# Optimization experiments

Measured on AMD Instinct MI355X. Metric: run time of the kernel, lower is better.

## Reference

```python
import jax, jax.numpy as jnp
import numpy as np

B, N, M, K = 8, 4096, 32, 72
D = 6 + K
W_REG, W_CLS = 3.0, 1.0
SIMOTA_Q = 4
IOU_LEN = 15.0
EPS = 1e-12
BIG = 100000.0


def setup_inputs() -> dict:
    key = jax.random.key(0)
    k1, k2, k3, k4, k5, k6 = jax.random.split(key, 6)
    preds = jax.random.normal(k1, (B, N, D), jnp.float32)
    # pred x-offsets in pixel range
    preds = preds.at[..., 6:].set(jax.random.uniform(k2, (B, N, K), jnp.float32, 0.0, 800.0))
    tgt = jax.random.normal(k3, (B, M, D), jnp.float32) * 0.1
    tgt = tgt.at[..., 1].set(jax.random.randint(k4, (B, M), 0, 2).astype(jnp.float32))
    tgt = tgt.at[..., 2:5].set(jax.random.uniform(k5, (B, M, 3), jnp.float32) * jnp.array([800.0, 320.0, 3.14159], jnp.float32))
    # target x-offsets, some out-of-range -> invalid points
    tgt = tgt.at[..., 6:].set(jax.random.uniform(k6, (B, M, K), jnp.float32, -50.0, 850.0))
    masks = jax.random.uniform(jax.random.fold_in(key, 7), (B, M)) > 0.2
    return {"preds": preds, "targets": tgt, "masks": masks, "img_w": 800, "img_h": 320}


def _focal_cost(cls_logits, gt_labels, alpha=0.25, gamma=2.0):
    # cls_logits [B,N,2], gt_labels [B,M] int -> [B,N,M]
    p = jax.nn.sigmoid(cls_logits)
    neg = -jnp.log(1.0 - p + EPS) * (1.0 - alpha) * p ** gamma
    pos = -jnp.log(p + EPS) * alpha * (1.0 - p) ** gamma
    diff = pos - neg  # [B,N,2]
    idx = jnp.broadcast_to(gt_labels[:, None, :], (gt_labels.shape[0], cls_logits.shape[1], gt_labels.shape[1]))
    return jnp.take_along_axis(diff, idx, axis=2)


def _pairwise_line_iou(pred_x, tgt_x, img_w, length=IOU_LEN):
    # pred_x [B,N,K], tgt_x [B,M,K] -> [B,N,M]
    p = pred_x[:, :, None, :]
    t = tgt_x[:, None, :, :]
    ovr = jnp.minimum(p + length, t + length) - jnp.maximum(p - length, t - length)
    union = jnp.maximum(p + length, t + length) - jnp.minimum(p - length, t - length)
    invalid = (t < 0) | (t >= img_w)
    ovr = jnp.where(invalid, 0.0, ovr)
    union = jnp.where(invalid, 0.0, union)
    return ovr.sum(-1) / (union.sum(-1) + 1e-9)


def _cost(preds, targets, masks, img_w):
    # -> cost [B,N,M]
    pred_dx = preds[..., 6:]
    tgt_dx = targets[..., 6:]
    invalid = (tgt_dx < 0) | (tgt_dx >= img_w)  # [B,M,K]
    lengths = jnp.maximum((~invalid).sum(-1), 1)  # [B,M]
    d = jnp.abs(tgt_dx[:, None, :, :] - pred_dx[:, :, None, :])  # [B,N,M,K]
    d = jnp.where(invalid[:, None, :, :], 0.0, d)
    distances = d.sum(-1) / lengths[:, None, :].astype(preds.dtype)  # [B,N,M]
    max_d = jnp.maximum(distances.max(axis=(1, 2), keepdims=True), 1e-6)
    dist_s = 1.0 - distances / max_d + 0.01
    xy = jnp.linalg.norm(preds[:, :, None, 2:4] - targets[:, None, :, 2:4], axis=-1)
    xy_s = 1.0 - xy / jnp.maximum(xy.max(axis=(1, 2), keepdims=True), 1e-6) + 0.01
    th = jnp.abs(preds[:, :, None, 4] - targets[:, None, :, 4])
    th_s = 1.0 - th / jnp.maximum(th.max(axis=(1, 2), keepdims=True), 1e-6) + 0.01
    cls_cost = _focal_cost(preds[..., :2], targets[..., 1].astype(jnp.int32))
    cost = -((dist_s * xy_s * th_s) ** 2) * W_REG + cls_cost * W_CLS
    return jnp.where(masks[:, None, :], cost, BIG)


def _assign(cost, iou, masks):
    b, n, m = cost.shape
    ious = jnp.where(masks[:, None, :], iou, 0.0)
    ious = jnp.maximum(ious, 0.0)
    n_cand = min(SIMOTA_Q, n)
    topk_ious, _ = jax.lax.top_k(jnp.swapaxes(ious, 1, 2), n_cand)  # [B,M,q]
    dynamic_ks = jnp.clip(topk_ious.sum(-1).astype(jnp.int32), 1, n)  # [B,M]
    # since line-iou <= 1, dynamic_ks <= SIMOTA_Q -> static max_k = n_cand
    max_k = n_cand
    _, topk_idx = jax.lax.top_k(-jnp.swapaxes(cost, 1, 2), max_k)  # [B,M,max_k] smallest costs
    k_mask = jnp.arange(max_k)[None, None, :] < dynamic_ks[:, :, None]  # [B,M,max_k]
    bi = jnp.arange(b)[:, None, None]
    mi = jnp.arange(m)[None, :, None]
    mmT = jnp.zeros((b, m, n), cost.dtype).at[bi, mi, topk_idx].set(k_mask.astype(cost.dtype))
    matching = jnp.swapaxes(mmT, 1, 2)  # [B,N,M]
    matching = jnp.where(masks[:, None, :], matching, 0.0)
    matched_gt = matching.sum(-1)  # [B,N]
    conflict = matched_gt > 1.0
    cost_inf = jnp.where(matching == 0.0, jnp.inf, cost)
    min_idx = jnp.argmin(cost_inf, axis=2)  # [B,N]
    one_hot = jax.nn.one_hot(min_idx, m, dtype=cost.dtype)
    matching = jnp.where(conflict[:, :, None], one_hot, matching)
    assigned = matching.sum(-1) > 0.0
    matched_t = jnp.argmax(matching, axis=2)
    matched_t = jnp.where(assigned, matched_t, -1)
    return assigned, matched_t


def reference(preds, targets, masks, img_w, img_h):
    cost = _cost(preds, targets, masks, img_w)
    iou = _pairwise_line_iou(preds[..., 6:], targets[..., 6:], img_w)
    return _assign(cost, iou, masks)
```

## Files before the change

### kernel.cpp

```cpp
#include <hip/hip_runtime.h>
#include <stdint.h>

#define BB 8
#define NN 4096
#define MM 32
#define KK 72
#define DD 78
#define PAD 76

static constexpr float EPSF = 1e-12f;

__device__ inline bool getmask(const void* masks, int flag, int i) {
  if (flag) return ((const unsigned char*)masks)[i] != 0;
  return ((const int*)masks)[i] != 0;
}

__device__ inline unsigned long long packkey(float c, int m) {
  unsigned u = __float_as_uint(c);
  unsigned k = ((int)u < 0) ? ~u : (u ^ 0x80000000u);
  return ((unsigned long long)k << 32) | (unsigned)m;
}

__global__ __launch_bounds__(256) void k_pairs(
    const float* __restrict__ preds, const float* __restrict__ tgts,
    const int* __restrict__ imgw_p, const unsigned char* __restrict__ masks_raw,
    float* __restrict__ sadA, float4* __restrict__ pc4, float* __restrict__ cls,
    float* __restrict__ part, unsigned* __restrict__ mmask,
    unsigned long long* __restrict__ cmin, int* __restrict__ flag) {
  __shared__ __align__(16) float t_xs[MM][PAD];
  __shared__ __align__(16) float am_s[MM][PAD];
  __shared__ __align__(16) float px_s[32][PAD];
  __shared__ float pc_s[32][4];
  __shared__ float t_cx[MM], t_cy[MM], t_th[MM], t_len[MM];
  __shared__ float redv[4][3];

  const int b = blockIdx.x >> 7;
  const int n0 = (blockIdx.x & 127) << 5;
  const int tid = threadIdx.x;
  const float imgw = (float)(*imgw_p);

  if (tid < 32) {
    mmask[blockIdx.x * 32 + tid] = 0u;
    cmin[blockIdx.x * 32 + tid] = ~0ull;
  }
  if (blockIdx.x == 0 && tid < 64) {
    int i = tid * 4;
    bool nz = false;
#pragma unroll
    for (int j = 1; j < 4; ++j)
      if (masks_raw[i + j] != 0) nz = true;
    unsigned long long bal = __ballot(nz);
    if (tid == 0) *flag = (bal != 0ull) ? 1 : 0;
  }

  for (int idx = tid; idx < MM * DD; idx += 256) {
    int m = idx / DD, j = idx - m * DD;
    float v = tgts[((size_t)b * MM + m) * DD + j];
    if (j >= 6) t_xs[m][j - 6] = v;
    else if (j == 2) t_cx[m] = v;
    else if (j == 3) t_cy[m] = v;
    else if (j == 4) t_th[m] = v;
  }
  for (int idx = tid; idx < 32 * KK; idx += 256) {
    int ni = idx / KK, k = idx - ni * KK;
    px_s[ni][k] = preds[((size_t)b * NN + (n0 + ni)) * DD + 6 + k];
  }
  if (tid < 96) {
    int ni = tid / 3, c = tid - ni * 3;
    pc_s[ni][c] = preds[((size_t)b * NN + (n0 + ni)) * DD + 2 + c];
  }
  if (tid >= 128 && tid < 192) {
    int q = tid - 128;
    int ni = q >> 1, c = q & 1;
    float lg = preds[((size_t)b * NN + (n0 + ni)) * DD + c];
    float pp = 1.0f / (1.0f + expf(-lg));
    float neg = -logf(1.0f - pp + EPSF) * 0.75f * (pp * pp);
    float pos = -logf(pp + EPSF) * 0.25f * ((1.0f - pp) * (1.0f - pp));
    cls[((size_t)b * NN + (n0 + ni)) * 2 + c] = pos - neg;
  }
  __syncthreads();
  if (tid < 32)
    pc4[(size_t)b * NN + n0 + tid] =
        make_float4(pc_s[tid][0], pc_s[tid][1], pc_s[tid][2], 0.0f);
  for (int idx = tid; idx < MM * KK; idx += 256) {
    int m = idx / KK, k = idx - m * KK;
    float t = t_xs[m][k];
    am_s[m][k] = (t >= 0.0f && t < imgw) ? 1.0f : 0.0f;
  }
  __syncthreads();
  if (tid < MM) {
    float V = 0.f;
    for (int k = 0; k < KK; ++k) V += am_s[tid][k];
    t_len[tid] = (V > 0.f) ? V : 1.0f;
  }
  __syncthreads();

  const int m = tid >> 3;
  const int ni = tid & 7;

  float sad0 = 0.f, sad1 = 0.f, sad2 = 0.f, sad3 = 0.f;
  const float4* trow = reinterpret_cast<const float4*>(&t_xs[m][0]);
  const float4* arow = reinterpret_cast<const float4*>(&am_s[m][0]);
  const float4* p0 = reinterpret_cast<const float4*>(&px_s[ni][0]);
  const float4* p1 = reinterpret_cast<const float4*>(&px_s[ni + 8][0]);
  const float4* p2 = reinterpret_cast<const float4*>(&px_s[ni + 16][0]);
  const float4* p3 = reinterpret_cast<const float4*>(&px_s[ni + 24][0]);
#define STEP(T, A, Q, S) S = fmaf(fabsf((T) - (Q)), (A), S)
#pragma unroll
  for (int q = 0; q < KK / 4; ++q) {
    float4 t4 = trow[q], a4 = arow[q];
    float4 q0 = p0[q], q1 = p1[q], q2 = p2[q], q3 = p3[q];
    STEP(t4.x, a4.x, q0.x, sad0); STEP(t4.y, a4.y, q0.y, sad0);
    STEP(t4.z, a4.z, q0.z, sad0); STEP(t4.w, a4.w, q0.w, sad0);
    STEP(t4.x, a4.x, q1.x, sad1); STEP(t4.y, a4.y, q1.y, sad1);
    STEP(t4.z, a4.z, q1.z, sad1); STEP(t4.w, a4.w, q1.w, sad1);
    STEP(t4.x, a4.x, q2.x, sad2); STEP(t4.y, a4.y, q2.y, sad2);
    STEP(t4.z, a4.z, q2.z, sad2); STEP(t4.w, a4.w, q2.w, sad2);
    STEP(t4.x, a4.x, q3.x, sad3); STEP(t4.y, a4.y, q3.y, sad3);
    STEP(t4.z, a4.z, q3.z, sad3); STEP(t4.w, a4.w, q3.w, sad3);
  }
#undef STEP

  float md = 0.f, mxy = 0.f, mth = 0.f;
#pragma unroll
  for (int j = 0; j < 4; ++j) {
    int nrow = ni + 8 * j;
    float sad = (j == 0) ? sad0 : (j == 1) ? sad1 : (j == 2) ? sad2 : sad3;
    float dval = sad / t_len[m];
    float dx = pc_s[nrow][0] - t_cx[m], dy = pc_s[nrow][1] - t_cy[m];
    float xyv = sqrtf(fmaf(dx, dx, dy * dy));
    float thv = fabsf(pc_s[nrow][2] - t_th[m]);
    sadA[((size_t)(b * MM + m)) * NN + n0 + nrow] = sad;
    md = fmaxf(md, dval); mxy = fmaxf(mxy, xyv); mth = fmaxf(mth, thv);
  }

  for (int off = 32; off; off >>= 1) {
    md = fmaxf(md, __shfl_down(md, off));
    mxy = fmaxf(mxy, __shfl_down(mxy, off));
    mth = fmaxf(mth, __shfl_down(mth, off));
  }
  if ((tid & 63) == 0) {
    int w = tid >> 6;
    redv[w][0] = md; redv[w][1] = mxy; redv[w][2] = mth;
  }
  __syncthreads();
  if (tid == 0) {
    float a0 = fmaxf(fmaxf(redv[0][0], redv[1][0]), fmaxf(redv[2][0], redv[3][0]));
    float a1 = fmaxf(fmaxf(redv[0][1], redv[1][1]), fmaxf(redv[2][1], redv[3][1]));
    float a2 = fmaxf(fmaxf(redv[0][2], redv[1][2]), fmaxf(redv[2][2], redv[3][2]));
    part[(size_t)blockIdx.x * 3 + 0] = a0;
    part[(size_t)blockIdx.x * 3 + 1] = a1;
    part[(size_t)blockIdx.x * 3 + 2] = a2;
  }
}

__global__ __launch_bounds__(1024) void k_assign(
    const float* __restrict__ sadA, const float4* __restrict__ pc4,
    const float* __restrict__ cls, const float* __restrict__ tgts,
    const int* __restrict__ imgw_p, const float* __restrict__ part,
    const void* __restrict__ masks, const int* __restrict__ flag,
    unsigned* __restrict__ mmask, unsigned long long* __restrict__ cmin) {
  const int b = blockIdx.x >> 5;
  const int m = blockIdx.x & 31;
  if (!getmask(masks, *flag, b * MM + m)) return;

  const int tid = threadIdx.x;
  __shared__ float wred[6];
  __shared__ float bcast[3];
  __shared__ float scal[8];

  if (tid < 384) {
    int g = tid >> 7;
    int e = tid & 127;
    float v = part[((size_t)(b * 128 + e)) * 3 + g];
    for (int off = 32; off; off >>= 1) v = fmaxf(v, __shfl_down(v, off));
    if ((tid & 63) == 0) wred[tid >> 6] = v;
  }
  if (tid >= 896 && tid < 960) {
    int lane = tid - 896;
    const float* trow = tgts + ((size_t)(b * MM + m)) * DD;
    const float imgw = (float)(*imgw_p);
    float t0 = trow[6 + lane];
    int c = (t0 >= 0.0f && t0 < imgw) ? 1 : 0;
    if (lane < KK - 64) {
      float t1 = trow[6 + 64 + lane];
      c += (t1 >= 0.0f && t1 < imgw) ? 1 : 0;
    }
    for (int off = 32; off; off >>= 1) c += __shfl_down(c, off);
    if (lane == 0) {
      float V = (float)c;
      scal[3] = (V > 0.f) ? V : 1.0f;
      scal[4] = 30.0f * V;
    }
  }
  if (tid == 1023) {
    const float* trow = tgts + ((size_t)(b * MM + m)) * DD;
    scal[0] = trow[2]; scal[1] = trow[3]; scal[2] = trow[4];
  }
  __syncthreads();
  if (tid == 0) {
    bcast[0] = fmaxf(wred[0], wred[1]);
    bcast[1] = fmaxf(wred[2], wred[3]);
    bcast[2] = fmaxf(wred[4], wred[5]);
  }
  __syncthreads();

  const float maxd = fmaxf(bcast[0], 1e-6f);
  const float maxxy = fmaxf(bcast[1], 1e-6f);
  const float maxth = fmaxf(bcast[2], 1e-6f);
  const float tcx = scal[0], tcy = scal[1], tth = scal[2];
  const float len = scal[3], v30 = scal[4];
  const int label = (int)tgts[((size_t)b * MM + m) * DD + 1];

  const int n0 = tid << 2;
  float4 s4 = *reinterpret_cast<const float4*>(sadA + ((size_t)(b * MM + m)) * NN + n0);
  const float4* pcb = pc4 + (size_t)b * NN + n0;
  float4 q0 = pcb[0], q1 = pcb[1], q2 = pcb[2], q3 = pcb[3];
  const float4* cbase = reinterpret_cast<const float4*>(cls + ((size_t)b * NN + n0) * 2);
  float4 c0 = cbase[0], c1 = cbase[1];

  float se[4] = {s4.x, s4.y, s4.z, s4.w};
  float cxe[4] = {q0.x, q1.x, q2.x, q3.x};
  float cye[4] = {q0.y, q1.y, q2.y, q3.y};
  float the[4] = {q0.z, q1.z, q2.z, q3.z};
  float clv[4] = {label ? c0.y : c0.x, label ? c0.w : c0.z,
                  label ? c1.y : c1.x, label ? c1.w : c1.z};

  float cc[4]; int ci[4]; float vv[4];
#pragma unroll
  for (int e = 0; e < 4; ++e) {
    float sad = se[e];
    float dval = sad / len;
    float dx = cxe[e] - tcx, dy = cye[e] - tcy;
    float xyv = sqrtf(fmaf(dx, dx, dy * dy));
    float thv = fabsf(the[e] - tth);
    float iv = (v30 - sad) / ((v30 + sad) + 1e-9f);
    float ds = (1.0f - dval / maxd) + 0.01f;
    float xs = (1.0f - xyv / maxxy) + 0.01f;
    float ts = (1.0f - thv / maxth) + 0.01f;
    float r = (ds * xs) * ts;
    cc[e] = -(r * r) * 3.0f + clv[e] * 1.0f;
    ci[e] = n0 + e;
    vv[e] = fmaxf(iv, 0.0f);
  }

  __shared__ float ls_c[64];  __shared__ int ls_ci[64];
  __shared__ float ls_v[64];  __shared__ int ls_vi[64];

  const int wid = tid >> 6, lane = tid & 63;
  unsigned usedC = 0, usedV = 0;
  float wcv[4]; int wci[4]; float wvv[4]; int wvi[4];

#pragma unroll
  for (int r = 0; r < 4; ++r) {
    float bv = 3e38f; int bi = 0x7fffffff; int be = -1;
#pragma unroll
    for (int e = 0; e < 4; ++e)
      if (!((usedC >> e) & 1) && (cc[e] < bv || (cc[e] == bv && ci[e] < bi))) {
        bv = cc[e]; bi = ci[e]; be = e;
      }
    float v = bv; int i = bi;
#pragma unroll
    for (int off = 32; off; off >>= 1) {
      float ov = __shfl_xor(v, off); int oi = __shfl_xor(i, off);
      if (ov < v || (ov == v && oi < i)) { v = ov; i = oi; }
    }
    if (be >= 0 && i == bi) usedC |= 1u << be;
    wcv[r] = v; wci[r] = i;

    float bw = -1.0f; int bj = 0x7fffffff; int bf = -1;
#pragma unroll
    for (int e = 0; e < 4; ++e)
      if (!((usedV >> e) & 1) && (vv[e] > bw || (vv[e] == bw && ci[e] < bj))) {
        bw = vv[e]; bj = ci[e]; bf = e;
      }
    float w = bw; int j = bj;
#pragma unroll
    for (int off = 32; off; off >>= 1) {
      float ow = __shfl_xor(w, off); int oj = __shfl_xor(j, off);
      if (ow > w || (ow == w && oj < j)) { w = ow; j = oj; }
    }
    if (bf >= 0 && j == bj) usedV |= 1u << bf;
    wvv[r] = w; wvi[r] = j;
  }

  if (lane == 0) {
#pragma unroll
    for (int r = 0; r < 4; ++r) {
      ls_c[wid * 4 + r] = wcv[r]; ls_ci[wid * 4 + r] = wci[r];
      ls_v[wid * 4 + r] = wvv[r]; ls_vi[wid * 4 + r] = wvi[r];
    }
  }
  __syncthreads();

  if (tid < 64) {
    float c = ls_c[tid]; int i = ls_ci[tid];
    float w = ls_v[tid]; int j = ls_vi[tid];
    int gidx[4]; float gcst[4]; float gsum = 0.0f;
#pragma unroll
    for (int r = 0; r < 4; ++r) {
      float v = c; int vi = i;
#pragma unroll
      for (int off = 32; off; off >>= 1) {
        float ov = __shfl_xor(v, off); int oi = __shfl_xor(vi, off);
        if (ov < v || (ov == v && oi < vi)) { v = ov; vi = oi; }
      }
      if (i == vi) c = 3e38f;
      gidx[r] = vi; gcst[r] = v;

      float u = w; int ui = j;
#pragma unroll
      for (int off = 32; off; off >>= 1) {
        float ou = __shfl_xor(u, off); int oi = __shfl_xor(ui, off);
        if (ou > u || (ou == u && oi < ui)) { u = ou; ui = oi; }
      }
      if (j == ui) w = -1.0f;
      gsum += u;
    }
    if (tid == 0) {
      int k = (int)gsum;
      if (k < 1) k = 1;
      if (k > 4) k = 4;
      for (int s = 0; s < k; ++s) {
        atomicOr(&mmask[(size_t)b * NN + gidx[s]], 1u << m);
        atomicMin(&cmin[(size_t)b * NN + gidx[s]], packkey(gcst[s], m));
      }
    }
  }
}

__global__ __launch_bounds__(256) void k_final(
    const unsigned* __restrict__ mmask,
    const unsigned long long* __restrict__ cmin, int* __restrict__ out) {
  int idx = blockIdx.x * 256 + threadIdx.x;
  if (idx >= BB * NN) return;
  unsigned mm = mmask[idx];
  int pc = __popc(mm);
  int t = pc ? (int)(unsigned)(cmin[idx] & 0xFFFFFFFFull) : -1;
  out[idx] = pc ? 1 : 0;
  out[BB * NN + idx] = t;
}

extern "C" void kernel_launch(void* const* d_in, const int* in_sizes, int n_in,
                              void* d_out, int out_size, void* d_ws, size_t ws_size,
                              hipStream_t stream) {
  const float* preds = (const float*)d_in[0];
  const float* tgts = (const float*)d_in[1];
  const void* masks = d_in[2];
  const int* imgw = (const int*)d_in[3];

  char* ws = (char*)d_ws;
  float* sadA = (float*)ws;
  char* p = ws + (size_t)BB * MM * NN * sizeof(float);
  float4* pc4 = (float4*)p;
  p += (size_t)BB * NN * sizeof(float4);
  float* cls = (float*)p;
  p += (size_t)BB * NN * 2 * sizeof(float);
  float* part = (float*)p;
  p += (size_t)1024 * 3 * sizeof(float);
  unsigned* mmask = (unsigned*)p;
  p += (size_t)BB * NN * sizeof(unsigned);
  unsigned long long* cmin = (unsigned long long*)p;
  p += (size_t)BB * NN * sizeof(unsigned long long);
  int* flag = (int*)p;

  k_pairs<<<dim3(BB * 128), dim3(256), 0, stream>>>(
      preds, tgts, imgw, (const unsigned char*)masks,
      sadA, pc4, cls, part, mmask, cmin, flag);
  k_assign<<<dim3(BB * MM), dim3(1024), 0, stream>>>(
      sadA, pc4, cls, tgts, imgw, part, masks, flag, mmask, cmin);
  k_final<<<dim3((BB * NN + 255) / 256), dim3(256), 0, stream>>>(
      mmask, cmin, (int*)d_out);
}
```

Measured before the change: 44.02 us.

## Register-tile pairwise SAD as 4x4 per thread with larger pred tiles

The pairwise SAD kernel now processes 64 predictions per block with 128 threads, and each thread computes a 4x4 tile of (target, prediction) pairs instead of 1x4. This cuts shared-memory loads per FMA and halves the number of blocks. The validity mask is built while loading targets, which removes one barrier. The per-block max partials shrink to 64 per batch, so the assign kernel reduces them in a single wave per component and drops one barrier. In exchange the kernel launches fewer, larger blocks (512 blocks of 2 waves), which lowers occupancy and uses more registers per thread.

Result: slower. 49.42 us (+12.3%).

```diff
diff --git a/kernel.cpp b/kernel.cpp
--- a/kernel.cpp
+++ b/kernel.cpp
@@ -21,7 +21,7 @@
   return ((unsigned long long)k << 32) | (unsigned)m;
 }
 
-__global__ __launch_bounds__(256) void k_pairs(
+__global__ __launch_bounds__(128) void k_pairs(
     const float* __restrict__ preds, const float* __restrict__ tgts,
     const int* __restrict__ imgw_p, const unsigned char* __restrict__ masks_raw,
     float* __restrict__ sadA, float4* __restrict__ pc4, float* __restrict__ cls,
@@ -29,19 +29,19 @@
     unsigned long long* __restrict__ cmin, int* __restrict__ flag) {
   __shared__ __align__(16) float t_xs[MM][PAD];
   __shared__ __align__(16) float am_s[MM][PAD];
-  __shared__ __align__(16) float px_s[32][PAD];
-  __shared__ float pc_s[32][4];
+  __shared__ __align__(16) float px_s[64][PAD];
+  __shared__ float pc_s[64][4];
   __shared__ float t_cx[MM], t_cy[MM], t_th[MM], t_len[MM];
-  __shared__ float redv[4][3];
-
-  const int b = blockIdx.x >> 7;
-  const int n0 = (blockIdx.x & 127) << 5;
+  __shared__ float redv[2][3];
+
+  const int b = blockIdx.x >> 6;
+  const int n0 = (blockIdx.x & 63) << 6;
   const int tid = threadIdx.x;
   const float imgw = (float)(*imgw_p);
 
-  if (tid < 32) {
-    mmask[blockIdx.x * 32 + tid] = 0u;
-    cmin[blockIdx.x * 32 + tid] = ~0ull;
+  if (tid < 64) {
+    mmask[blockIdx.x * 64 + tid] = 0u;
+    cmin[blockIdx.x * 64 + tid] = ~0ull;
   }
   if (blockIdx.x == 0 && tid < 64) {
     int i = tid * 4;
@@ -53,25 +53,26 @@
     if (tid == 0) *flag = (bal != 0ull) ? 1 : 0;
   }
 
-  for (int idx = tid; idx < MM * DD; idx += 256) {
+  for (int idx = tid; idx < MM * DD; idx += 128) {
     int m = idx / DD, j = idx - m * DD;
     float v = tgts[((size_t)b * MM + m) * DD + j];
-    if (j >= 6) t_xs[m][j - 6] = v;
-    else if (j == 2) t_cx[m] = v;
+    if (j >= 6) {
+      t_xs[m][j - 6] = v;
+      am_s[m][j - 6] = (v >= 0.0f && v < imgw) ? 1.0f : 0.0f;
+    } else if (j == 2) t_cx[m] = v;
     else if (j == 3) t_cy[m] = v;
     else if (j == 4) t_th[m] = v;
   }
-  for (int idx = tid; idx < 32 * KK; idx += 256) {
+  for (int idx = tid; idx < 64 * KK; idx += 128) {
     int ni = idx / KK, k = idx - ni * KK;
     px_s[ni][k] = preds[((size_t)b * NN + (n0 + ni)) * DD + 6 + k];
   }
-  if (tid < 96) {
-    int ni = tid / 3, c = tid - ni * 3;
+  for (int idx = tid; idx < 64 * 3; idx += 128) {
+    int ni = idx / 3, c = idx - ni * 3;
     pc_s[ni][c] = preds[((size_t)b * NN + (n0 + ni)) * DD + 2 + c];
   }
-  if (tid >= 128 && tid < 192) {
-    int q = tid - 128;
-    int ni = q >> 1, c = q & 1;
+  {
+    int ni = tid >> 1, c = tid & 1;
     float lg = preds[((size_t)b * NN + (n0 + ni)) * DD + c];
     float pp = 1.0f / (1.0f + expf(-lg));
     float neg = -logf(1.0f - pp + EPSF) * 0.75f * (pp * pp);
@@ -79,15 +80,9 @@
     cls[((size_t)b * NN + (n0 + ni)) * 2 + c] = pos - neg;
   }
   __syncthreads();
-  if (tid < 32)
+  if (tid < 64)
     pc4[(size_t)b * NN + n0 + tid] =
         make_float4(pc_s[tid][0], pc_s[tid][1], pc_s[tid][2], 0.0f);
-  for (int idx = tid; idx < MM * KK; idx += 256) {
-    int m = idx / KK, k = idx - m * KK;
-    float t = t_xs[m][k];
-    am_s[m][k] = (t >= 0.0f && t < imgw) ? 1.0f : 0.0f;
-  }
-  __syncthreads();
   if (tid < MM) {
     float V = 0.f;
     for (int k = 0; k < KK; ++k) V += am_s[tid][k];
@@ -95,44 +90,63 @@
   }
   __syncthreads();
 
-  const int m = tid >> 3;
-  const int ni = tid & 7;
-
-  float sad0 = 0.f, sad1 = 0.f, sad2 = 0.f, sad3 = 0.f;
-  const float4* trow = reinterpret_cast<const float4*>(&t_xs[m][0]);
-  const float4* arow = reinterpret_cast<const float4*>(&am_s[m][0]);
-  const float4* p0 = reinterpret_cast<const float4*>(&px_s[ni][0]);
-  const float4* p1 = reinterpret_cast<const float4*>(&px_s[ni + 8][0]);
-  const float4* p2 = reinterpret_cast<const float4*>(&px_s[ni + 16][0]);
-  const float4* p3 = reinterpret_cast<const float4*>(&px_s[ni + 24][0]);
-#define STEP(T, A, Q, S) S = fmaf(fabsf((T) - (Q)), (A), S)
-#pragma unroll
+  const int mt = tid >> 4;
+  const int nt = tid & 15;
+  const int mbase = mt << 2;
+
+  const float4* t0r = reinterpret_cast<const float4*>(&t_xs[mbase + 0][0]);
+  const float4* t1r = reinterpret_cast<const float4*>(&t_xs[mbase + 1][0]);
+  const float4* t2r = reinterpret_cast<const float4*>(&t_xs[mbase + 2][0]);
+  const float4* t3r = reinterpret_cast<const float4*>(&t_xs[mbase + 3][0]);
+  const float4* a0r = reinterpret_cast<const float4*>(&am_s[mbase + 0][0]);
+  const float4* a1r = reinterpret_cast<const float4*>(&am_s[mbase + 1][0]);
+  const float4* a2r = reinterpret_cast<const float4*>(&am_s[mbase + 2][0]);
+  const float4* a3r = reinterpret_cast<const float4*>(&am_s[mbase + 3][0]);
+  const float4* p0r = reinterpret_cast<const float4*>(&px_s[nt][0]);
+  const float4* p1r = reinterpret_cast<const float4*>(&px_s[nt + 16][0]);
+  const float4* p2r = reinterpret_cast<const float4*>(&px_s[nt + 32][0]);
+  const float4* p3r = reinterpret_cast<const float4*>(&px_s[nt + 48][0]);
+
+  float s00 = 0.f, s01 = 0.f, s02 = 0.f, s03 = 0.f;
+  float s10 = 0.f, s11 = 0.f, s12 = 0.f, s13 = 0.f;
+  float s20 = 0.f, s21 = 0.f, s22 = 0.f, s23 = 0.f;
+  float s30 = 0.f, s31 = 0.f, s32 = 0.f, s33 = 0.f;
+
+#define ST(S, T, A, P)                       \
+  S = fmaf(fabsf((T).x - (P).x), (A).x, S);  \
+  S = fmaf(fabsf((T).y - (P).y), (A).y, S);  \
+  S = fmaf(fabsf((T).z - (P).z), (A).z, S);  \
+  S = fmaf(fabsf((T).w - (P).w), (A).w, S);
+#pragma unroll 3
   for (int q = 0; q < KK / 4; ++q) {
-    float4 t4 = trow[q], a4 = arow[q];
-    float4 q0 = p0[q], q1 = p1[q], q2 = p2[q], q3 = p3[q];
-    STEP(t4.x, a4.x, q0.x, sad0); STEP(t4.y, a4.y, q0.y, sad0);
-    STEP(t4.z, a4.z, q0.z, sad0); STEP(t4.w, a4.w, q0.w, sad0);
-    STEP(t4.x, a4.x, q1.x, sad1); STEP(t4.y, a4.y, q1.y, sad1);
-    STEP(t4.z, a4.z, q1.z, sad1); STEP(t4.w, a4.w, q1.w, sad1);
-    STEP(t4.x, a4.x, q2.x, sad2); STEP(t4.y, a4.y, q2.y, sad2);
-    STEP(t4.z, a4.z, q2.z, sad2); STEP(t4.w, a4.w, q2.w, sad2);
-    STEP(t4.x, a4.x, q3.x, sad3); STEP(t4.y, a4.y, q3.y, sad3);
-    STEP(t4.z, a4.z, q3.z, sad3); STEP(t4.w, a4.w, q3.w, sad3);
-  }
-#undef STEP
+    float4 T0 = t0r[q], A0 = a0r[q], T1 = t1r[q], A1 = a1r[q];
+    float4 T2 = t2r[q], A2 = a2r[q], T3 = t3r[q], A3 = a3r[q];
+    float4 P0 = p0r[q], P1 = p1r[q], P2 = p2r[q], P3 = p3r[q];
+    ST(s00, T0, A0, P0) ST(s01, T0, A0, P1) ST(s02, T0, A0, P2) ST(s03, T0, A0, P3)
+    ST(s10, T1, A1, P0) ST(s11, T1, A1, P1) ST(s12, T1, A1, P2) ST(s13, T1, A1, P3)
+    ST(s20, T2, A2, P0) ST(s21, T2, A2, P1) ST(s22, T2, A2, P2) ST(s23, T2, A2, P3)
+    ST(s30, T3, A3, P0) ST(s31, T3, A3, P1) ST(s32, T3, A3, P2) ST(s33, T3, A3, P3)
+  }
+#undef ST
 
   float md = 0.f, mxy = 0.f, mth = 0.f;
-#pragma unroll
-  for (int j = 0; j < 4; ++j) {
-    int nrow = ni + 8 * j;
-    float sad = (j == 0) ? sad0 : (j == 1) ? sad1 : (j == 2) ? sad2 : sad3;
-    float dval = sad / t_len[m];
-    float dx = pc_s[nrow][0] - t_cx[m], dy = pc_s[nrow][1] - t_cy[m];
-    float xyv = sqrtf(fmaf(dx, dx, dy * dy));
-    float thv = fabsf(pc_s[nrow][2] - t_th[m]);
-    sadA[((size_t)(b * MM + m)) * NN + n0 + nrow] = sad;
-    md = fmaxf(md, dval); mxy = fmaxf(mxy, xyv); mth = fmaxf(mth, thv);
-  }
+#define FIN(S, MI, NJ)                                                        \
+  {                                                                           \
+    float sad = S;                                                            \
+    int mi = mbase + (MI);                                                    \
+    int nr = nt + 16 * (NJ);                                                  \
+    float dval = sad / t_len[mi];                  \
+    float dx = pc_s[nr][0] - t_cx[mi], dy = pc_s[nr][1] - t_cy[mi];           \
+    float xyv = sqrtf(fmaf(dx, dx, dy * dy));  \
+    float thv = fabsf(pc_s[nr][2] - t_th[mi]);                                \
+    sadA[((size_t)(b * MM + mi)) * NN + n0 + nr] = sad;                       \
+    md = fmaxf(md, dval); mxy = fmaxf(mxy, xyv); mth = fmaxf(mth, thv);       \
+  }
+  FIN(s00, 0, 0) FIN(s01, 0, 1) FIN(s02, 0, 2) FIN(s03, 0, 3)
+  FIN(s10, 1, 0) FIN(s11, 1, 1) FIN(s12, 1, 2) FIN(s13, 1, 3)
+  FIN(s20, 2, 0) FIN(s21, 2, 1) FIN(s22, 2, 2) FIN(s23, 2, 3)
+  FIN(s30, 3, 0) FIN(s31, 3, 1) FIN(s32, 3, 2) FIN(s33, 3, 3)
+#undef FIN
 
   for (int off = 32; off; off >>= 1) {
     md = fmaxf(md, __shfl_down(md, off));
@@ -145,12 +159,9 @@
   }
   __syncthreads();
   if (tid == 0) {
-    float a0 = fmaxf(fmaxf(redv[0][0], redv[1][0]), fmaxf(redv[2][0], redv[3][0]));
-    float a1 = fmaxf(fmaxf(redv[0][1], redv[1][1]), fmaxf(redv[2][1], redv[3][1]));
-    float a2 = fmaxf(fmaxf(redv[0][2], redv[1][2]), fmaxf(redv[2][2], redv[3][2]));
-    part[(size_t)blockIdx.x * 3 + 0] = a0;
-    part[(size_t)blockIdx.x * 3 + 1] = a1;
-    part[(size_t)blockIdx.x * 3 + 2] = a2;
+    part[(size_t)blockIdx.x * 3 + 0] = fmaxf(redv[0][0], redv[1][0]);
+    part[(size_t)blockIdx.x * 3 + 1] = fmaxf(redv[0][1], redv[1][1]);
+    part[(size_t)blockIdx.x * 3 + 2] = fmaxf(redv[0][2], redv[1][2]);
   }
 }
 
@@ -165,16 +176,14 @@
   if (!getmask(masks, *flag, b * MM + m)) return;
 
   const int tid = threadIdx.x;
-  __shared__ float wred[6];
   __shared__ float bcast[3];
   __shared__ float scal[8];
 
-  if (tid < 384) {
-    int g = tid >> 7;
-    int e = tid & 127;
-    float v = part[((size_t)(b * 128 + e)) * 3 + g];
+  if (tid < 192) {
+    int g = tid >> 6, e = tid & 63;
+    float v = part[((size_t)(b * 64 + e)) * 3 + g];
     for (int off = 32; off; off >>= 1) v = fmaxf(v, __shfl_down(v, off));
-    if ((tid & 63) == 0) wred[tid >> 6] = v;
+    if ((tid & 63) == 0) bcast[g] = v;
   }
   if (tid >= 896 && tid < 960) {
     int lane = tid - 896;
@@ -196,12 +205,6 @@
   if (tid == 1023) {
     const float* trow = tgts + ((size_t)(b * MM + m)) * DD;
     scal[0] = trow[2]; scal[1] = trow[3]; scal[2] = trow[4];
-  }
-  __syncthreads();
-  if (tid == 0) {
-    bcast[0] = fmaxf(wred[0], wred[1]);
-    bcast[1] = fmaxf(wred[2], wred[3]);
-    bcast[2] = fmaxf(wred[4], wred[5]);
   }
   __syncthreads();
 
@@ -364,7 +367,7 @@
   p += (size_t)BB * NN * sizeof(unsigned long long);
   int* flag = (int*)p;
 
-  k_pairs<<<dim3(BB * 128), dim3(256), 0, stream>>>(
+  k_pairs<<<dim3(BB * 64), dim3(128), 0, stream>>>(
       preds, tgts, imgw, (const unsigned char*)masks,
       sadA, pc4, cls, part, mmask, cmin, flag);
   k_assign<<<dim3(BB * MM), dim3(1024), 0, stream>>>(
```
